# Optimization experiments

Hardware: AMD Instinct MI355X
Metric: run time of the kernel (lower is better)

## Reference

```python
import jax, jax.numpy as jnp
import numpy as np

STRIDE = 2

def setup_inputs() -> dict:
    key = jax.random.key(0)
    x = jax.random.normal(key, (8, 256, 112, 112), dtype=jnp.float32)
    return {"x": x}

def reference(x) -> jnp.ndarray:
    # Equivalent to conv_transpose2d with a depthwise kernel that has a single 1
    # at position (0,0): each input value is copied to the top-left of each
    # stride x stride block of the output; all other positions are zero.
    B, C, H, W = x.shape
    s = STRIDE
    out = jnp.zeros((B, C, H * s, W * s), dtype=x.dtype)
    out = out.at[:, :, ::s, ::s].set(x)
    return out
```

## Files before the change

### kernel.cpp

```cpp
#include <hip/hip_runtime.h>


__global__ __launch_bounds__(256) void unpool_x2dbg(
    const float2* __restrict__ in, float* __restrict__ out,
    unsigned n, unsigned half)
{
    const unsigned t = blockIdx.x * blockDim.x + threadIdx.x;
    if (t >= n) return;

    {
        const unsigned u = t;
        const unsigned r = u / 56u, j = u - r * 56u;
        const float2 v = in[u];
        float* b = out + 448u * r + 4u * j;
        *reinterpret_cast<float4*>(b)       = make_float4(v.x, 0.f, v.y, 0.f);
        *reinterpret_cast<float4*>(b + 224) = make_float4(0.f, 0.f, 0.f, 0.f);
    }

    {
        const unsigned u = (t >= half) ? (t - half) : (t + half);
        const unsigned r = u / 56u, j = u - r * 56u;
        const float2 v = in[u];
        float* b = out + 448u * r + 4u * j;
        *reinterpret_cast<float4*>(b)       = make_float4(v.x, 0.f, v.y, 0.f);
        *reinterpret_cast<float4*>(b + 224) = make_float4(0.f, 0.f, 0.f, 0.f);
    }
}

extern "C" void kernel_launch(void* const* d_in, const int* in_sizes, int n_in,
                              void* d_out, int out_size, void* d_ws, size_t ws_size,
                              hipStream_t stream)
{
    const float2* x = (const float2*)d_in[0];
    float* out      = (float*)d_out;

    unsigned n    = (unsigned)in_sizes[0] / 2u;
    unsigned half = n / 2u;
    int block     = 256;
    int grid      = (int)((n + block - 1) / block);

    unpool_x2dbg<<<grid, block, 0, stream>>>(x, out, n, half);
}
```

Before: 553.7 us.

## Replace duplicated per-thread writes with persistent grid-stride unrolled sweep

The old kernel had every thread process both its own element and a mirrored element half the array away. That wrote every output element twice and read every input twice. The new kernel launches a fixed grid of 1792x256 threads, each processing four elements per iteration in a strided sweep with precomputed row offsets, so every element is written once. It relies on the stride being an exact multiple of the 56-wide row pair (ROWADV constant), which ties the indexing to this shape, and a tail loop handles the remainder.

```diff
diff --git a/kernel.cpp b/kernel.cpp
--- a/kernel.cpp
+++ b/kernel.cpp
@@ -1,29 +1,55 @@
 #include <hip/hip_runtime.h>
 
 
-__global__ __launch_bounds__(256) void unpool_x2dbg(
-    const float2* __restrict__ in, float* __restrict__ out,
-    unsigned n, unsigned half)
+#define GRID   1792
+#define BLOCK  256
+#define TSTR   (GRID * BLOCK)
+#define KU     4
+#define STEP   (TSTR * KU)
+#define ROWADV (448u * 8192u)
+
+__global__ __launch_bounds__(256) void unpool_sweep(
+    const float2* __restrict__ in, float* __restrict__ out, unsigned n)
 {
-    const unsigned t = blockIdx.x * blockDim.x + threadIdx.x;
-    if (t >= n) return;
+    const unsigned t  = blockIdx.x * blockDim.x + threadIdx.x;
+    const unsigned rt = t / 56u;
+    const unsigned jt = t - rt * 56u;
 
-    {
-        const unsigned u = t;
-        const unsigned r = u / 56u, j = u - r * 56u;
-        const float2 v = in[u];
-        float* b = out + 448u * r + 4u * j;
-        *reinterpret_cast<float4*>(b)       = make_float4(v.x, 0.f, v.y, 0.f);
-        *reinterpret_cast<float4*>(b + 224) = make_float4(0.f, 0.f, 0.f, 0.f);
+    float* const bt = out + 448u * rt + 4u * jt;
+    const float4 z4 = make_float4(0.f, 0.f, 0.f, 0.f);
+
+    const unsigned nsteps = n / STEP;
+
+    for (unsigned i = 0; i < nsteps; ++i) {
+        const unsigned q = i * KU;
+
+        const float2 v0 = in[(q + 0u) * TSTR + t];
+        const float2 v1 = in[(q + 1u) * TSTR + t];
+        const float2 v2 = in[(q + 2u) * TSTR + t];
+        const float2 v3 = in[(q + 3u) * TSTR + t];
+
+        float* b0 = bt + (q + 0u) * ROWADV;
+        float* b1 = bt + (q + 1u) * ROWADV;
+        float* b2 = bt + (q + 2u) * ROWADV;
+        float* b3 = bt + (q + 3u) * ROWADV;
+
+        *reinterpret_cast<float4*>(b0 + 224) = z4;
+        *reinterpret_cast<float4*>(b1 + 224) = z4;
+        *reinterpret_cast<float4*>(b2 + 224) = z4;
+        *reinterpret_cast<float4*>(b3 + 224) = z4;
+
+        *reinterpret_cast<float4*>(b0) = make_float4(v0.x, 0.f, v0.y, 0.f);
+        *reinterpret_cast<float4*>(b1) = make_float4(v1.x, 0.f, v1.y, 0.f);
+        *reinterpret_cast<float4*>(b2) = make_float4(v2.x, 0.f, v2.y, 0.f);
+        *reinterpret_cast<float4*>(b3) = make_float4(v3.x, 0.f, v3.y, 0.f);
     }
 
-    {
-        const unsigned u = (t >= half) ? (t - half) : (t + half);
+    for (unsigned u = nsteps * STEP + t; u < n; u += TSTR) {
+        const float2 v = in[u];
         const unsigned r = u / 56u, j = u - r * 56u;
-        const float2 v = in[u];
         float* b = out + 448u * r + 4u * j;
+        *reinterpret_cast<float4*>(b + 224) = z4;
         *reinterpret_cast<float4*>(b)       = make_float4(v.x, 0.f, v.y, 0.f);
-        *reinterpret_cast<float4*>(b + 224) = make_float4(0.f, 0.f, 0.f, 0.f);
     }
 }
 
@@ -34,10 +60,7 @@
     const float2* x = (const float2*)d_in[0];
     float* out      = (float*)d_out;
 
-    unsigned n    = (unsigned)in_sizes[0] / 2u;
-    unsigned half = n / 2u;
-    int block     = 256;
-    int grid      = (int)((n + block - 1) / block);
+    unsigned n = (unsigned)in_sizes[0] / 2u;
 
-    unpool_x2dbg<<<grid, block, 0, stream>>>(x, out, n, half);
+    unpool_sweep<<<GRID, BLOCK, 0, stream>>>(x, out, n);
 }
```

Measured after the change: 477.3 us. 1.16x faster.
